# Kernel optimization log

Hardware: AMD Instinct MI355X
Metric: run time of the kernel (lower is better)

Reference implementation:

```python
import jax, jax.numpy as jnp
import numpy as np

B = 2048        # batch
C = 64          # args.embed_size (channel dim; attention runs over this axis)
N = 11          # spatial rows per window
D = 11          # args.hsi_windowSize
SA = N * D      # args.size_SA = 121, Linear in/out size
HID = 128       # args.hid_router
NUM_PATH = 4    # num_out_path


def setup_inputs() -> dict:
    key = jax.random.key(0)
    ks = jax.random.split(key, 12)
    w = lambda k, shape: (jax.random.normal(k, shape, dtype=jnp.float32) * 0.05)
    return {
        "lidar": jax.random.normal(ks[0], (B, C, N, D), dtype=jnp.float32),
        "hsi": jax.random.normal(ks[1], (B, C, N, D), dtype=jnp.float32),
        # Cross_Self_attention linears (shared module, used in both directions)
        "Wq": w(ks[2], (SA, SA)), "bq": jnp.zeros((SA,), jnp.float32),
        "Wk": w(ks[3], (SA, SA)), "bk": jnp.zeros((SA,), jnp.float32),
        "Wv": w(ks[4], (SA, SA)), "bv": jnp.zeros((SA,), jnp.float32),
        # Router MLP: Linear(2C, HID) -> ReLU -> Linear(HID, NUM_PATH) -> softmax
        "Wr1": w(ks[5], (2 * C, HID)), "br1": jnp.zeros((HID,), jnp.float32),
        "Wr2": w(ks[6], (HID, NUM_PATH)), "br2": jnp.zeros((NUM_PATH,), jnp.float32),
        # 1x1 Conv2d(2C -> C): pure channel mixing
        "Wc": w(ks[7], (C, 2 * C)), "bc": jnp.zeros((C,), jnp.float32),
    }


def reference(lidar, hsi, Wq, bq, Wk, bk, Wv, bv, Wr1, br1, Wr2, br2, Wc, bc):
    def cross_sa(x, y):
        # x, y: [B, C, SA]; Linear acts on last dim (size_SA)
        q = x @ Wq.T + bq                                   # [B, C, SA]
        k = x @ Wk.T + bk                                   # [B, C, SA]
        v = y @ Wv.T + bv                                   # [B, C, SA]
        scores = jnp.einsum('bhs,bgs->bhg', q, k)           # [B, C, C] attn over channels
        probs = jax.nn.softmax(scores, axis=-1)
        # custom: attn @ (Q * V) elementwise gate instead of attn @ V
        return jnp.einsum('bhg,bgs->bhs', probs, q * v)     # [B, C, SA]
        # dropout(0.5) is identity in eval mode

    # router on channel-concat of raw inputs
    pooled = jnp.concatenate([lidar, hsi], axis=1).mean(axis=(2, 3))   # [B, 2C]
    path_prob = jax.nn.softmax(jax.nn.relu(pooled @ Wr1 + br1) @ Wr2 + br2, axis=-1)

    l = lidar.reshape(B, C, SA)
    h = hsi.reshape(B, C, SA)
    h_emb = cross_sa(l, h).reshape(B, C, N, D)
    l_emb = cross_sa(h, l).reshape(B, C, N, D)

    cat = jnp.concatenate([l_emb, h_emb], axis=1)                       # [B, 2C, N, D]
    emb = jnp.einsum('oc,bchw->bohw', Wc, cat) + bc[None, :, None, None]
    return (emb, path_prob)
```

## Files before the change

### kernel.cpp

```cpp
#include <hip/hip_runtime.h>

#define NB 2048
#define SA 121
#define EMB_TOTAL (NB * 64 * SA)

typedef short bf16x8 __attribute__((ext_vector_type(8)));
typedef float f32x4  __attribute__((ext_vector_type(4)));

__device__ __forceinline__ short f2bf(float f) {
    union { float f; unsigned u; } v; v.f = f;
    unsigned r = (v.u + 0x7fffu + ((v.u >> 16) & 1u)) >> 16;
    return (short)r;
}
__device__ __forceinline__ float bf2f(short s) {
    union { unsigned u; float f; } v; v.u = ((unsigned)(unsigned short)s) << 16;
    return v.f;
}

#define MFMA(a, b, c) __builtin_amdgcn_mfma_f32_16x16x32_bf16((a), (b), (c), 0, 0, 0)

__global__ void convert_weights(const float* __restrict__ Wq, const float* __restrict__ Wk,
                                const float* __restrict__ Wv, const float* __restrict__ Wc,
                                short* __restrict__ ws) {
    int i = blockIdx.x * 256 + threadIdx.x;
    if (i < 49152) {
        int m = i / 16384;
        const float* W = (m == 0) ? Wq : ((m == 1) ? Wk : Wv);
        int j = i & 16383;
        int r = j >> 7, c = j & 127;
        float v = (r < SA && c < SA) ? W[r * SA + c] : 0.f;
        ws[i] = f2bf(v);
    } else {
        int j = i - 49152;
        ws[i] = f2bf(Wc[j]);
    }
}

__launch_bounds__(256, 2)
__global__ void fused_kernel(const float* __restrict__ lidar, const float* __restrict__ hsi,
                             const float* __restrict__ bq, const float* __restrict__ bk,
                             const float* __restrict__ bv,
                             const float* __restrict__ Wr1, const float* __restrict__ br1,
                             const float* __restrict__ Wr2, const float* __restrict__ br2,
                             const float* __restrict__ bc,
                             const short* __restrict__ wsb, float* __restrict__ out) {
    __shared__ __align__(16) short sA[64 * 136];
    __shared__ __align__(16) short sB[64 * 136];
    __shared__ __align__(16) short sC[64 * 136];
    __shared__ __align__(16) short sD[128 * 72];
    __shared__ __align__(16) short sE[64 * 72];
    __shared__ float sR[260];

    const int tid  = threadIdx.x;
    const int b    = blockIdx.x;
    const int lane = tid & 63;
    const int wid  = tid >> 6;
    const int l16  = lane & 15;
    const int g16  = lane >> 4;

    const short* WQ = wsb;
    const short* WK = wsb + 16384;
    const short* WV = wsb + 32768;
    const short* WC = wsb + 49152;

    bf16x8 wqf[2][4], wkf[2][4], wvf[2][4];
    #pragma unroll
    for (int nn = 0; nn < 2; ++nn) {
        const int rw = ((wid * 2 + nn) * 16 + l16) * 128 + g16 * 8;
        #pragma unroll
        for (int k0 = 0; k0 < 4; ++k0) {
            wqf[nn][k0] = *(const bf16x8*)&WQ[rw + k0 * 32];
            wkf[nn][k0] = *(const bf16x8*)&WK[rw + k0 * 32];
            wvf[nn][k0] = *(const bf16x8*)&WV[rw + k0 * 32];
        }
    }
    bf16x8 wcf[2][2];
    {
        const int rw = (wid * 16 + l16) * 128 + g16 * 8;
        #pragma unroll
        for (int cb = 0; cb < 2; ++cb)
            #pragma unroll
            for (int k0 = 0; k0 < 2; ++k0)
                wcf[cb][k0] = *(const bf16x8*)&WC[rw + cb * 64 + k0 * 32];
    }
    float bqv[2], bkv[2], bvv2[2];
    #pragma unroll
    for (int nn = 0; nn < 2; ++nn) {
        int sc_ = (wid * 2 + nn) * 16 + l16;
        bool ok = sc_ < SA;
        bqv[nn]  = ok ? bq[sc_] : 0.f;
        bkv[nn]  = ok ? bk[sc_] : 0.f;
        bvv2[nn] = ok ? bv[sc_] : 0.f;
    }

    {
        const int row = wid * 16 + l16;
        const float* gA = lidar + (size_t)b * 7744 + row * 121;
        const float* gB = hsi   + (size_t)b * 7744 + row * 121;
        float rsA = 0.f, rsB = 0.f;
        #pragma unroll
        for (int k0 = 0; k0 < 4; ++k0) {
            const int c0 = k0 * 32 + g16 * 8;
            bf16x8 a, h;
            if (c0 == 120) {
                float xa = gA[120], xb = gB[120];
                rsA += xa; rsB += xb;
                a[0] = f2bf(xa); h[0] = f2bf(xb);
                #pragma unroll
                for (int j = 1; j < 8; ++j) { a[j] = 0; h[j] = 0; }
            } else {
                #pragma unroll
                for (int j = 0; j < 8; ++j) {
                    float xa = gA[c0 + j], xb = gB[c0 + j];
                    rsA += xa; rsB += xb;
                    a[j] = f2bf(xa); h[j] = f2bf(xb);
                }
            }
            *(bf16x8*)&sA[row * 136 + c0] = a;
            *(bf16x8*)&sB[row * 136 + c0] = h;
        }
        rsA += __shfl_xor(rsA, 16, 64); rsA += __shfl_xor(rsA, 32, 64);
        rsB += __shfl_xor(rsB, 16, 64); rsB += __shfl_xor(rsB, 32, 64);
        if (g16 == 0) { sR[row] = rsA * (1.f / 121.f); sR[64 + row] = rsB * (1.f / 121.f); }
    }
    __syncthreads();

    f32x4 eacc[8];
    #pragma unroll
    for (int n = 0; n < 8; ++n) eacc[n] = (f32x4){0.f, 0.f, 0.f, 0.f};

    #pragma unroll 1
    for (int dir = 0; dir < 2; ++dir) {
        const short* Xqk = dir ? sB : sA;
        const short* Xv  = dir ? sA : sB;
        const int cb = dir ? 0 : 1;

        #pragma unroll 1
        for (int m = 0; m < 4; ++m) {
            bf16x8 afr[4];
            #pragma unroll
            for (int k0 = 0; k0 < 4; ++k0)
                afr[k0] = *(const bf16x8*)&Xqk[(m * 16 + l16) * 136 + k0 * 32 + g16 * 8];
            f32x4 qa[2], ka[2];
            qa[0] = (f32x4){0,0,0,0}; qa[1] = (f32x4){0,0,0,0};
            ka[0] = (f32x4){0,0,0,0}; ka[1] = (f32x4){0,0,0,0};
            #pragma unroll
            for (int k0 = 0; k0 < 4; ++k0)
                #pragma unroll
                for (int nn = 0; nn < 2; ++nn) {
                    qa[nn] = MFMA(afr[k0], wqf[nn][k0], qa[nn]);
                    ka[nn] = MFMA(afr[k0], wkf[nn][k0], ka[nn]);
                }
            #pragma unroll
            for (int nn = 0; nn < 2; ++nn) {
                int sc_ = (wid * 2 + nn) * 16 + l16;
                #pragma unroll
                for (int r = 0; r < 4; ++r) {
                    int row = m * 16 + g16 * 4 + r;
                    sC[row * 136 + sc_] = f2bf(qa[nn][r] + bqv[nn]);
                    sD[row * 136 + sc_] = f2bf(ka[nn][r] + bkv[nn]);
                }
            }
        }
        __syncthreads();

        {
            f32x4 sc4[4];
            #pragma unroll
            for (int n = 0; n < 4; ++n) sc4[n] = (f32x4){0,0,0,0};
            #pragma unroll
            for (int k0 = 0; k0 < 4; ++k0) {
                bf16x8 afr = *(const bf16x8*)&sC[(wid * 16 + l16) * 136 + k0 * 32 + g16 * 8];
                #pragma unroll
                for (int n = 0; n < 4; ++n) {
                    bf16x8 bfr = *(const bf16x8*)&sD[(n * 16 + l16) * 136 + k0 * 32 + g16 * 8];
                    sc4[n] = MFMA(afr, bfr, sc4[n]);
                }
            }
            #pragma unroll
            for (int r = 0; r < 4; ++r) {
                float mx = fmaxf(fmaxf(sc4[0][r], sc4[1][r]), fmaxf(sc4[2][r], sc4[3][r]));
                #pragma unroll
                for (int off = 1; off < 16; off <<= 1) mx = fmaxf(mx, __shfl_xor(mx, off, 64));
                float e0 = exp2f((sc4[0][r] - mx) * 1.44269504f);
                float e1 = exp2f((sc4[1][r] - mx) * 1.44269504f);
                float e2 = exp2f((sc4[2][r] - mx) * 1.44269504f);
                float e3 = exp2f((sc4[3][r] - mx) * 1.44269504f);
                float sum = e0 + e1 + e2 + e3;
                #pragma unroll
                for (int off = 1; off < 16; off <<= 1) sum += __shfl_xor(sum, off, 64);
                float inv = 1.f / sum;
                int crow = wid * 16 + g16 * 4 + r;
                sE[(0 * 16 + l16) * 72 + crow] = f2bf(e0 * inv);
                sE[(1 * 16 + l16) * 72 + crow] = f2bf(e1 * inv);
                sE[(2 * 16 + l16) * 72 + crow] = f2bf(e2 * inv);
                sE[(3 * 16 + l16) * 72 + crow] = f2bf(e3 * inv);
            }
        }
        __syncthreads();

        {
            #pragma unroll 1
            for (int m = 0; m < 4; ++m) {
                bf16x8 afr[4];
                #pragma unroll
                for (int k0 = 0; k0 < 4; ++k0)
                    afr[k0] = *(const bf16x8*)&Xv[(m * 16 + l16) * 136 + k0 * 32 + g16 * 8];
                f32x4 va[2];
                va[0] = (f32x4){0,0,0,0}; va[1] = (f32x4){0,0,0,0};
                #pragma unroll
                for (int k0 = 0; k0 < 4; ++k0)
                    #pragma unroll
                    for (int nn = 0; nn < 2; ++nn)
                        va[nn] = MFMA(afr[k0], wvf[nn][k0], va[nn]);
                #pragma unroll
                for (int nn = 0; nn < 2; ++nn) {
                    int sc_ = (wid * 2 + nn) * 16 + l16;
                    #pragma unroll
                    for (int r = 0; r < 4; ++r) {
                        int c = m * 16 + g16 * 4 + r;
                        float qv = bf2f(sC[c * 136 + sc_]);
                        sD[sc_ * 72 + c] = f2bf((va[nn][r] + bvv2[nn]) * qv);
                    }
                }
            }
            f32x4 macc[4];
            #pragma unroll
            for (int n = 0; n < 4; ++n) macc[n] = (f32x4){0,0,0,0};
            #pragma unroll
            for (int k0 = 0; k0 < 2; ++k0)
                #pragma unroll
                for (int n = 0; n < 4; ++n) {
                    bf16x8 bfr = *(const bf16x8*)&sE[(n * 16 + l16) * 72 + k0 * 32 + g16 * 8];
                    macc[n] = MFMA(wcf[cb][k0], bfr, macc[n]);
                }
            __syncthreads();
            #pragma unroll
            for (int n = 0; n < 4; ++n)
                #pragma unroll
                for (int r = 0; r < 4; ++r) {
                    int o = wid * 16 + g16 * 4 + r;
                    sE[o * 72 + n * 16 + l16] = f2bf(macc[n][r]);
                }
        }
        __syncthreads();

        #pragma unroll
        for (int k0 = 0; k0 < 2; ++k0) {
            bf16x8 afr = *(const bf16x8*)&sE[(wid * 16 + l16) * 72 + k0 * 32 + g16 * 8];
            #pragma unroll
            for (int n = 0; n < 8; ++n) {
                bf16x8 bfr = *(const bf16x8*)&sD[(n * 16 + l16) * 72 + k0 * 32 + g16 * 8];
                eacc[n] = MFMA(afr, bfr, eacc[n]);
            }
        }
        __syncthreads();
    }

    float* eo = out + (size_t)b * 7744;
    {
        float bcv[4];
        #pragma unroll
        for (int r = 0; r < 4; ++r) bcv[r] = bc[wid * 16 + g16 * 4 + r];
        #pragma unroll
        for (int n = 0; n < 8; ++n) {
            int s = n * 16 + l16;
            if (s < SA) {
                #pragma unroll
                for (int r = 0; r < 4; ++r) {
                    int o = wid * 16 + g16 * 4 + r;
                    eo[o * 121 + s] = eacc[n][r] + bcv[r];
                }
            }
        }
    }

    if (tid < 128) {
        float a0 = 0.f, a1 = 0.f, a2 = 0.f, a3 = 0.f;
        for (int c = 0; c < 128; c += 4) {
            a0 += sR[c]     * Wr1[(c)     * 128 + tid];
            a1 += sR[c + 1] * Wr1[(c + 1) * 128 + tid];
            a2 += sR[c + 2] * Wr1[(c + 2) * 128 + tid];
            a3 += sR[c + 3] * Wr1[(c + 3) * 128 + tid];
        }
        sR[128 + tid] = fmaxf((a0 + a1) + (a2 + a3) + br1[tid], 0.f);
    }
    __syncthreads();
    if (tid < 4) {
        float a0 = 0.f, a1 = 0.f, a2 = 0.f, a3 = 0.f;
        for (int h = 0; h < 128; h += 4) {
            a0 += sR[128 + h]     * Wr2[(h)     * 4 + tid];
            a1 += sR[128 + h + 1] * Wr2[(h + 1) * 4 + tid];
            a2 += sR[128 + h + 2] * Wr2[(h + 2) * 4 + tid];
            a3 += sR[128 + h + 3] * Wr2[(h + 3) * 4 + tid];
        }
        sR[256 + tid] = (a0 + a1) + (a2 + a3) + br2[tid];
    }
    __syncthreads();
    if (tid < 4) {
        float m = fmaxf(fmaxf(sR[256], sR[257]), fmaxf(sR[258], sR[259]));
        float e = __expf(sR[256 + tid] - m);
        float s = 0.f;
        for (int p = 0; p < 4; ++p) s += __expf(sR[256 + p] - m);
        out[EMB_TOTAL + b * 4 + tid] = e / s;
    }
}

extern "C" void kernel_launch(void* const* d_in, const int* in_sizes, int n_in,
                              void* d_out, int out_size, void* d_ws, size_t ws_size,
                              hipStream_t stream) {
    const float* lidar = (const float*)d_in[0];
    const float* hsi   = (const float*)d_in[1];
    const float* Wq  = (const float*)d_in[2];  const float* bq  = (const float*)d_in[3];
    const float* Wk  = (const float*)d_in[4];  const float* bk  = (const float*)d_in[5];
    const float* Wv  = (const float*)d_in[6];  const float* bv  = (const float*)d_in[7];
    const float* Wr1 = (const float*)d_in[8];  const float* br1 = (const float*)d_in[9];
    const float* Wr2 = (const float*)d_in[10]; const float* br2 = (const float*)d_in[11];
    const float* Wc  = (const float*)d_in[12]; const float* bc  = (const float*)d_in[13];
    short* wsb = (short*)d_ws;
    float* out = (float*)d_out;

    hipLaunchKernelGGL(convert_weights, dim3(224), dim3(256), 0, stream, Wq, Wk, Wv, Wc, wsb);
    hipLaunchKernelGGL(fused_kernel, dim3(NB), dim3(256), 0, stream,
                       lidar, hsi, bq, bk, bv, Wr1, br1, Wr2, br2, bc, wsb, out);
}
```

Measured before the change: 114.5 us.

## Fold Wq·Wk into one precomputed matrix and drop K projection and bk

Precomputes Wq^T·Wk and Wk^T·bq in the weight-conversion kernel, so attention scores are computed as (X·A)·X^T plus a per-column bias term, with the bk-dependent row-constant terms dropped since softmax ignores them. Q is recomputed alongside V in the gating stage instead of being stored in shared memory, which removes one LDS buffer and its writes. The MFMA count stays similar, LDS usage drops, and the prep kernel does a small naive matmul each call; bf16 rounding of the fused matrix changes numerics slightly.

```diff
diff --git a/kernel.cpp b/kernel.cpp
--- a/kernel.cpp
+++ b/kernel.cpp
@@ -12,44 +12,48 @@
     unsigned r = (v.u + 0x7fffu + ((v.u >> 16) & 1u)) >> 16;
     return (short)r;
 }
-__device__ __forceinline__ float bf2f(short s) {
-    union { unsigned u; float f; } v; v.u = ((unsigned)(unsigned short)s) << 16;
-    return v.f;
-}
 
 #define MFMA(a, b, c) __builtin_amdgcn_mfma_f32_16x16x32_bf16((a), (b), (c), 0, 0, 0)
 
 __global__ void convert_weights(const float* __restrict__ Wq, const float* __restrict__ Wk,
                                 const float* __restrict__ Wv, const float* __restrict__ Wc,
-                                short* __restrict__ ws) {
+                                const float* __restrict__ bq, short* __restrict__ ws) {
     int i = blockIdx.x * 256 + threadIdx.x;
-    if (i < 49152) {
-        int m = i / 16384;
-        const float* W = (m == 0) ? Wq : ((m == 1) ? Wk : Wv);
-        int j = i & 16383;
-        int r = j >> 7, c = j & 127;
-        float v = (r < SA && c < SA) ? W[r * SA + c] : 0.f;
-        ws[i] = f2bf(v);
-    } else {
-        int j = i - 49152;
-        ws[i] = f2bf(Wc[j]);
+    if (i < 16384) {
+        int t = i >> 7, s = i & 127;
+        float acc = 0.f;
+        if (t < SA && s < SA)
+            for (int j = 0; j < SA; ++j) acc += Wq[j * SA + s] * Wk[j * SA + t];
+        ws[i] = f2bf(acc);
+    } else if (i < 32768) {
+        int j = i - 16384; int r = j >> 7, c = j & 127;
+        ws[i] = f2bf((r < SA && c < SA) ? Wq[r * SA + c] : 0.f);
+    } else if (i < 49152) {
+        int j = i - 32768; int r = j >> 7, c = j & 127;
+        ws[i] = f2bf((r < SA && c < SA) ? Wv[r * SA + c] : 0.f);
+    } else if (i < 57344) {
+        ws[i] = f2bf(Wc[i - 49152]);
+    } else if (i < 57472) {
+        int t = i - 57344;
+        float acc = 0.f;
+        if (t < SA)
+            for (int j = 0; j < SA; ++j) acc += bq[j] * Wk[j * SA + t];
+        ((float*)(ws + 57344))[t] = acc;
     }
 }
 
 __launch_bounds__(256, 2)
 __global__ void fused_kernel(const float* __restrict__ lidar, const float* __restrict__ hsi,
-                             const float* __restrict__ bq, const float* __restrict__ bk,
-                             const float* __restrict__ bv,
+                             const float* __restrict__ bq, const float* __restrict__ bv,
                              const float* __restrict__ Wr1, const float* __restrict__ br1,
                              const float* __restrict__ Wr2, const float* __restrict__ br2,
                              const float* __restrict__ bc,
                              const short* __restrict__ wsb, float* __restrict__ out) {
     __shared__ __align__(16) short sA[64 * 136];
     __shared__ __align__(16) short sB[64 * 136];
-    __shared__ __align__(16) short sC[64 * 136];
     __shared__ __align__(16) short sD[128 * 72];
     __shared__ __align__(16) short sE[64 * 72];
-    __shared__ float sR[260];
+    __shared__ float sR[388];
 
     const int tid  = threadIdx.x;
     const int b    = blockIdx.x;
@@ -58,19 +62,20 @@
     const int l16  = lane & 15;
     const int g16  = lane >> 4;
 
-    const short* WQ = wsb;
-    const short* WK = wsb + 16384;
+    const short* WA = wsb;
+    const short* WQ = wsb + 16384;
     const short* WV = wsb + 32768;
     const short* WC = wsb + 49152;
-
-    bf16x8 wqf[2][4], wkf[2][4], wvf[2][4];
+    const float* wvp = (const float*)(wsb + 57344);
+
+    bf16x8 wwa[2][4], wqf[2][4], wvf[2][4];
     #pragma unroll
     for (int nn = 0; nn < 2; ++nn) {
         const int rw = ((wid * 2 + nn) * 16 + l16) * 128 + g16 * 8;
         #pragma unroll
         for (int k0 = 0; k0 < 4; ++k0) {
+            wwa[nn][k0] = *(const bf16x8*)&WA[rw + k0 * 32];
             wqf[nn][k0] = *(const bf16x8*)&WQ[rw + k0 * 32];
-            wkf[nn][k0] = *(const bf16x8*)&WK[rw + k0 * 32];
             wvf[nn][k0] = *(const bf16x8*)&WV[rw + k0 * 32];
         }
     }
@@ -83,13 +88,12 @@
             for (int k0 = 0; k0 < 2; ++k0)
                 wcf[cb][k0] = *(const bf16x8*)&WC[rw + cb * 64 + k0 * 32];
     }
-    float bqv[2], bkv[2], bvv2[2];
+    float bqv[2], bvv2[2];
     #pragma unroll
     for (int nn = 0; nn < 2; ++nn) {
         int sc_ = (wid * 2 + nn) * 16 + l16;
         bool ok = sc_ < SA;
         bqv[nn]  = ok ? bq[sc_] : 0.f;
-        bkv[nn]  = ok ? bk[sc_] : 0.f;
         bvv2[nn] = ok ? bv[sc_] : 0.f;
     }
 
@@ -97,14 +101,14 @@
         const int row = wid * 16 + l16;
         const float* gA = lidar + (size_t)b * 7744 + row * 121;
         const float* gB = hsi   + (size_t)b * 7744 + row * 121;
-        float rsA = 0.f, rsB = 0.f;
+        float rsA = 0.f, rsB = 0.f, wA = 0.f, wB = 0.f;
         #pragma unroll
         for (int k0 = 0; k0 < 4; ++k0) {
             const int c0 = k0 * 32 + g16 * 8;
             bf16x8 a, h;
             if (c0 == 120) {
-                float xa = gA[120], xb = gB[120];
-                rsA += xa; rsB += xb;
+                float xa = gA[120], xb = gB[120], wv0 = wvp[120];
+                rsA += xa; rsB += xb; wA += xa * wv0; wB += xb * wv0;
                 a[0] = f2bf(xa); h[0] = f2bf(xb);
                 #pragma unroll
                 for (int j = 1; j < 8; ++j) { a[j] = 0; h[j] = 0; }
@@ -112,7 +116,9 @@
                 #pragma unroll
                 for (int j = 0; j < 8; ++j) {
                     float xa = gA[c0 + j], xb = gB[c0 + j];
+                    float wv0 = wvp[c0 + j];
                     rsA += xa; rsB += xb;
+                    wA += xa * wv0; wB += xb * wv0;
                     a[j] = f2bf(xa); h[j] = f2bf(xb);
                 }
             }
@@ -121,7 +127,14 @@
         }
         rsA += __shfl_xor(rsA, 16, 64); rsA += __shfl_xor(rsA, 32, 64);
         rsB += __shfl_xor(rsB, 16, 64); rsB += __shfl_xor(rsB, 32, 64);
-        if (g16 == 0) { sR[row] = rsA * (1.f / 121.f); sR[64 + row] = rsB * (1.f / 121.f); }
+        wA  += __shfl_xor(wA, 16, 64);  wA  += __shfl_xor(wA, 32, 64);
+        wB  += __shfl_xor(wB, 16, 64);  wB  += __shfl_xor(wB, 32, 64);
+        if (g16 == 0) {
+            sR[row] = rsA * (1.f / 121.f);
+            sR[64 + row] = rsB * (1.f / 121.f);
+            sR[128 + row] = wA;
+            sR[192 + row] = wB;
+        }
     }
     __syncthreads();
 
@@ -141,25 +154,19 @@
             #pragma unroll
             for (int k0 = 0; k0 < 4; ++k0)
                 afr[k0] = *(const bf16x8*)&Xqk[(m * 16 + l16) * 136 + k0 * 32 + g16 * 8];
-            f32x4 qa[2], ka[2];
-            qa[0] = (f32x4){0,0,0,0}; qa[1] = (f32x4){0,0,0,0};
-            ka[0] = (f32x4){0,0,0,0}; ka[1] = (f32x4){0,0,0,0};
-            #pragma unroll
-            for (int k0 = 0; k0 < 4; ++k0)
-                #pragma unroll
-                for (int nn = 0; nn < 2; ++nn) {
-                    qa[nn] = MFMA(afr[k0], wqf[nn][k0], qa[nn]);
-                    ka[nn] = MFMA(afr[k0], wkf[nn][k0], ka[nn]);
-                }
+            f32x4 ya[2];
+            ya[0] = (f32x4){0,0,0,0}; ya[1] = (f32x4){0,0,0,0};
+            #pragma unroll
+            for (int k0 = 0; k0 < 4; ++k0) {
+                ya[0] = MFMA(afr[k0], wwa[0][k0], ya[0]);
+                ya[1] = MFMA(afr[k0], wwa[1][k0], ya[1]);
+            }
             #pragma unroll
             for (int nn = 0; nn < 2; ++nn) {
                 int sc_ = (wid * 2 + nn) * 16 + l16;
                 #pragma unroll
-                for (int r = 0; r < 4; ++r) {
-                    int row = m * 16 + g16 * 4 + r;
-                    sC[row * 136 + sc_] = f2bf(qa[nn][r] + bqv[nn]);
-                    sD[row * 136 + sc_] = f2bf(ka[nn][r] + bkv[nn]);
-                }
+                for (int r = 0; r < 4; ++r)
+                    sD[(m * 16 + g16 * 4 + r) * 136 + sc_] = f2bf(ya[nn][r]);
             }
         }
         __syncthreads();
@@ -170,22 +177,27 @@
             for (int n = 0; n < 4; ++n) sc4[n] = (f32x4){0,0,0,0};
             #pragma unroll
             for (int k0 = 0; k0 < 4; ++k0) {
-                bf16x8 afr = *(const bf16x8*)&sC[(wid * 16 + l16) * 136 + k0 * 32 + g16 * 8];
+                bf16x8 afr = *(const bf16x8*)&sD[(wid * 16 + l16) * 136 + k0 * 32 + g16 * 8];
                 #pragma unroll
                 for (int n = 0; n < 4; ++n) {
-                    bf16x8 bfr = *(const bf16x8*)&sD[(n * 16 + l16) * 136 + k0 * 32 + g16 * 8];
+                    bf16x8 bfr = *(const bf16x8*)&Xqk[(n * 16 + l16) * 136 + k0 * 32 + g16 * 8];
                     sc4[n] = MFMA(afr, bfr, sc4[n]);
                 }
             }
+            float wg[4];
+            #pragma unroll
+            for (int n = 0; n < 4; ++n) wg[n] = sR[128 + dir * 64 + n * 16 + l16];
             #pragma unroll
             for (int r = 0; r < 4; ++r) {
-                float mx = fmaxf(fmaxf(sc4[0][r], sc4[1][r]), fmaxf(sc4[2][r], sc4[3][r]));
+                float s0 = sc4[0][r] + wg[0], s1 = sc4[1][r] + wg[1];
+                float s2 = sc4[2][r] + wg[2], s3 = sc4[3][r] + wg[3];
+                float mx = fmaxf(fmaxf(s0, s1), fmaxf(s2, s3));
                 #pragma unroll
                 for (int off = 1; off < 16; off <<= 1) mx = fmaxf(mx, __shfl_xor(mx, off, 64));
-                float e0 = exp2f((sc4[0][r] - mx) * 1.44269504f);
-                float e1 = exp2f((sc4[1][r] - mx) * 1.44269504f);
-                float e2 = exp2f((sc4[2][r] - mx) * 1.44269504f);
-                float e3 = exp2f((sc4[3][r] - mx) * 1.44269504f);
+                float e0 = exp2f((s0 - mx) * 1.44269504f);
+                float e1 = exp2f((s1 - mx) * 1.44269504f);
+                float e2 = exp2f((s2 - mx) * 1.44269504f);
+                float e3 = exp2f((s3 - mx) * 1.44269504f);
                 float sum = e0 + e1 + e2 + e3;
                 #pragma unroll
                 for (int off = 1; off < 16; off <<= 1) sum += __shfl_xor(sum, off, 64);
@@ -205,22 +217,32 @@
                 bf16x8 afr[4];
                 #pragma unroll
                 for (int k0 = 0; k0 < 4; ++k0)
+                    afr[k0] = *(const bf16x8*)&Xqk[(m * 16 + l16) * 136 + k0 * 32 + g16 * 8];
+                f32x4 qa[2];
+                qa[0] = (f32x4){0,0,0,0}; qa[1] = (f32x4){0,0,0,0};
+                #pragma unroll
+                for (int k0 = 0; k0 < 4; ++k0) {
+                    qa[0] = MFMA(afr[k0], wqf[0][k0], qa[0]);
+                    qa[1] = MFMA(afr[k0], wqf[1][k0], qa[1]);
+                }
+                #pragma unroll
+                for (int k0 = 0; k0 < 4; ++k0)
                     afr[k0] = *(const bf16x8*)&Xv[(m * 16 + l16) * 136 + k0 * 32 + g16 * 8];
                 f32x4 va[2];
                 va[0] = (f32x4){0,0,0,0}; va[1] = (f32x4){0,0,0,0};
                 #pragma unroll
-                for (int k0 = 0; k0 < 4; ++k0)
-                    #pragma unroll
-                    for (int nn = 0; nn < 2; ++nn)
-                        va[nn] = MFMA(afr[k0], wvf[nn][k0], va[nn]);
+                for (int k0 = 0; k0 < 4; ++k0) {
+                    va[0] = MFMA(afr[k0], wvf[0][k0], va[0]);
+                    va[1] = MFMA(afr[k0], wvf[1][k0], va[1]);
+                }
                 #pragma unroll
                 for (int nn = 0; nn < 2; ++nn) {
                     int sc_ = (wid * 2 + nn) * 16 + l16;
                     #pragma unroll
                     for (int r = 0; r < 4; ++r) {
                         int c = m * 16 + g16 * 4 + r;
-                        float qv = bf2f(sC[c * 136 + sc_]);
-                        sD[sc_ * 72 + c] = f2bf((va[nn][r] + bvv2[nn]) * qv);
+                        float g = (va[nn][r] + bvv2[nn]) * (qa[nn][r] + bqv[nn]);
+                        sD[sc_ * 72 + c] = f2bf(g);
                     }
                 }
             }
@@ -238,10 +260,8 @@
             #pragma unroll
             for (int n = 0; n < 4; ++n)
                 #pragma unroll
-                for (int r = 0; r < 4; ++r) {
-                    int o = wid * 16 + g16 * 4 + r;
-                    sE[o * 72 + n * 16 + l16] = f2bf(macc[n][r]);
-                }
+                for (int r = 0; r < 4; ++r)
+                    sE[(wid * 16 + g16 * 4 + r) * 72 + n * 16 + l16] = f2bf(macc[n][r]);
         }
         __syncthreads();
 
@@ -283,25 +303,25 @@
             a2 += sR[c + 2] * Wr1[(c + 2) * 128 + tid];
             a3 += sR[c + 3] * Wr1[(c + 3) * 128 + tid];
         }
-        sR[128 + tid] = fmaxf((a0 + a1) + (a2 + a3) + br1[tid], 0.f);
+        sR[256 + tid] = fmaxf((a0 + a1) + (a2 + a3) + br1[tid], 0.f);
     }
     __syncthreads();
     if (tid < 4) {
         float a0 = 0.f, a1 = 0.f, a2 = 0.f, a3 = 0.f;
         for (int h = 0; h < 128; h += 4) {
-            a0 += sR[128 + h]     * Wr2[(h)     * 4 + tid];
-            a1 += sR[128 + h + 1] * Wr2[(h + 1) * 4 + tid];
-            a2 += sR[128 + h + 2] * Wr2[(h + 2) * 4 + tid];
-            a3 += sR[128 + h + 3] * Wr2[(h + 3) * 4 + tid];
-        }
-        sR[256 + tid] = (a0 + a1) + (a2 + a3) + br2[tid];
+            a0 += sR[256 + h]     * Wr2[(h)     * 4 + tid];
+            a1 += sR[256 + h + 1] * Wr2[(h + 1) * 4 + tid];
+            a2 += sR[256 + h + 2] * Wr2[(h + 2) * 4 + tid];
+            a3 += sR[256 + h + 3] * Wr2[(h + 3) * 4 + tid];
+        }
+        sR[384 + tid] = (a0 + a1) + (a2 + a3) + br2[tid];
     }
     __syncthreads();
     if (tid < 4) {
-        float m = fmaxf(fmaxf(sR[256], sR[257]), fmaxf(sR[258], sR[259]));
-        float e = __expf(sR[256 + tid] - m);
+        float m = fmaxf(fmaxf(sR[384], sR[385]), fmaxf(sR[386], sR[387]));
+        float e = __expf(sR[384 + tid] - m);
         float s = 0.f;
-        for (int p = 0; p < 4; ++p) s += __expf(sR[256 + p] - m);
+        for (int p = 0; p < 4; ++p) s += __expf(sR[384 + p] - m);
         out[EMB_TOTAL + b * 4 + tid] = e / s;
     }
 }
@@ -312,7 +332,7 @@
     const float* lidar = (const float*)d_in[0];
     const float* hsi   = (const float*)d_in[1];
     const float* Wq  = (const float*)d_in[2];  const float* bq  = (const float*)d_in[3];
-    const float* Wk  = (const float*)d_in[4];  const float* bk  = (const float*)d_in[5];
+    const float* Wk  = (const float*)d_in[4];
     const float* Wv  = (const float*)d_in[6];  const float* bv  = (const float*)d_in[7];
     const float* Wr1 = (const float*)d_in[8];  const float* br1 = (const float*)d_in[9];
     const float* Wr2 = (const float*)d_in[10]; const float* br2 = (const float*)d_in[11];
@@ -320,7 +340,7 @@
     short* wsb = (short*)d_ws;
     float* out = (float*)d_out;
 
-    hipLaunchKernelGGL(convert_weights, dim3(224), dim3(256), 0, stream, Wq, Wk, Wv, Wc, wsb);
+    hipLaunchKernelGGL(convert_weights, dim3(225), dim3(256), 0, stream, Wq, Wk, Wv, Wc, bq, wsb);
     hipLaunchKernelGGL(fused_kernel, dim3(NB), dim3(256), 0, stream,
-                       lidar, hsi, bq, bk, bv, Wr1, br1, Wr2, br2, bc, wsb, out);
+                       lidar, hsi, bq, bv, Wr1, br1, Wr2, br2, bc, wsb, out);
 }
```

Result: slower. 138.6 us (+21.0%).
